# Optimization experiments

Measured on AMD Instinct MI355X. Metric: run time of the kernel, lower is better.

Reference implementation:

```python
import jax, jax.numpy as jnp
import numpy as np

B, S, D, H = 2, 2048, 1024, 16
HD = D // H  # 64


def setup_inputs() -> dict:
    key = jax.random.key(0)
    ks = jax.random.split(key, 10)
    inp = {
        "queries": jax.random.normal(ks[0], (B, S, D), dtype=jnp.float32),
        "keys": jax.random.normal(ks[1], (B, S, D), dtype=jnp.float32),
        "values": jax.random.normal(ks[2], (B, S, D), dtype=jnp.float32),
        "attention_mask": jax.random.randint(ks[3], (B, S), 0, 2, dtype=jnp.int32),
        # Linear params (torch nn.Linear: y = x @ W.T + b), scaled like default init
        "Wq": jax.random.normal(ks[4], (D, D), dtype=jnp.float32) / np.sqrt(D),
        "bq": jnp.zeros((D,), dtype=jnp.float32),
        "Wk": jax.random.normal(ks[5], (D, D), dtype=jnp.float32) / np.sqrt(D),
        "bk": jnp.zeros((D,), dtype=jnp.float32),
        "Wv": jax.random.normal(ks[6], (D, D), dtype=jnp.float32) / np.sqrt(D),
        "bv": jnp.zeros((D,), dtype=jnp.float32),
    }
    return inp


def _split_heads(x):
    # torch.chunk along last dim + stack(dim=1) == reshape + transpose
    b, s, d = x.shape
    return x.reshape(b, s, H, HD).transpose(0, 2, 1, 3)  # [B,H,S,hd]


def reference(queries, keys, values, attention_mask, Wq, bq, Wk, bk, Wv, bv):
    q = jax.nn.relu(queries @ Wq.T + bq)
    k = jax.nn.relu(keys @ Wk.T + bk)
    v = jax.nn.relu(values @ Wv.T + bv)
    qh, kh, vh = _split_heads(q), _split_heads(k), _split_heads(v)
    score = jnp.einsum("bhqd,bhkd->bhqk", qh, kh) / jnp.sqrt(jnp.float32(HD))
    # enc mask: [B,1,S,1] broadcast over key dim — masks whole query rows where mask==0
    row_mask = (attention_mask == 0)[:, None, :, None]
    score = jnp.where(row_mask, jnp.float32(-1e9), score)
    attn = jax.nn.softmax(score, axis=-1)
    a = jnp.einsum("bhqk,bhkd->bhqd", attn, vh)  # [B,H,S,hd]
    # faithful to original: permute(0,1,3,2) then reshape to (B,S,D)
    a = a.transpose(0, 1, 3, 2).reshape(q.shape[0], q.shape[1], q.shape[2])
    return a + queries
```

## Files before the change

### kernel.cpp

```cpp
#include <hip/hip_runtime.h>
#include <hip/hip_bf16.h>

#define DEV __device__ __forceinline__

typedef __attribute__((ext_vector_type(8))) short short8;
typedef __attribute__((ext_vector_type(4))) float f32x4;

#define MFMA16(a, b, c) __builtin_amdgcn_mfma_f32_16x16x32_bf16((a), (b), (c), 0, 0, 0)

static constexpr int B_ = 2, S_ = 2048, D_ = 1024, H_ = 16, HD_ = 64;
static constexpr long NX = (long)B_ * S_ * D_;
static constexpr long NW = (long)D_ * D_;

DEV short f2bf(float f) {
    __hip_bfloat16 h = __float2bfloat16(f);
    union { __hip_bfloat16 hh; short s; } u;
    u.hh = h;
    return u.s;
}

DEV float bf2f(short s) {
    union { float f; unsigned u; } x;
    x.u = ((unsigned)(unsigned short)s) << 16;
    return x.f;
}

DEV unsigned pk2(float a, float b) {
    union { float f; unsigned u; } ua, ub;
    ua.f = a; ub.f = b;
    return ((ua.u + 0x8000u) >> 16) | ((ub.u + 0x8000u) & 0xffff0000u);
}

DEV short8 ld8(const short* p) { return *(const short8*)p; }

DEV void gld16(const short* g, short* l) {
    __builtin_amdgcn_global_load_lds(
        (const __attribute__((address_space(1))) unsigned int*)g,
        (__attribute__((address_space(3))) unsigned int*)l, 16, 0, 0);
}

__global__ __launch_bounds__(256) void convert_all(
    const float* __restrict__ q, const float* __restrict__ k, const float* __restrict__ v,
    const float* __restrict__ wq, const float* __restrict__ wk, const float* __restrict__ wv,
    short* __restrict__ qb, short* __restrict__ kb, short* __restrict__ vb,
    short* __restrict__ wqb, short* __restrict__ wkb, short* __restrict__ wvb) {
    long tid = (long)blockIdx.x * 256 + threadIdx.x;
    long e = tid * 4;
    const float* src; short* dst; long off;
    if      (e < NX)            { src = q;  dst = qb;  off = e; }
    else if (e < 2*NX)          { src = k;  dst = kb;  off = e - NX; }
    else if (e < 3*NX)          { src = v;  dst = vb;  off = e - 2*NX; }
    else if (e < 3*NX + NW)     { src = wq; dst = wqb; off = e - 3*NX; }
    else if (e < 3*NX + 2*NW)   { src = wk; dst = wkb; off = e - 3*NX - NW; }
    else                        { src = wv; dst = wvb; off = e - 3*NX - 2*NW; }
    float4 f = *(const float4*)(src + off);
    short4 o;
    o.x = f2bf(f.x); o.y = f2bf(f.y); o.z = f2bf(f.z); o.w = f2bf(f.w);
    *(short4*)(dst + off) = o;
}

__global__ __launch_bounds__(256) void gemm_bias_relu(
    const short* __restrict__ X0, const short* __restrict__ X1, const short* __restrict__ X2,
    const short* __restrict__ W0, const short* __restrict__ W1, const short* __restrict__ W2,
    const float* __restrict__ b0, const float* __restrict__ b1, const float* __restrict__ b2,
    short* __restrict__ O0, short* __restrict__ O1, short* __restrict__ O2) {
    __shared__ short As[2][128 * 32];
    __shared__ short Bs[2][128 * 32];

    const int z = blockIdx.z;
    const short* X   = (z == 0) ? X0 : (z == 1) ? X1 : X2;
    const short* W   = (z == 0) ? W0 : (z == 1) ? W1 : W2;
    const float* bia = (z == 0) ? b0 : (z == 1) ? b1 : b2;
    short*       Out = (z == 0) ? O0 : (z == 1) ? O1 : O2;

    const int tid  = threadIdx.x;
    const int wid  = tid >> 6;
    const int lane = tid & 63;
    const int id   = lane & 15;
    const int quad = lane >> 4;
    const int m0 = blockIdx.y * 128;
    const int n0 = blockIdx.x * 128;
    const int wm = (wid >> 1) * 64;
    const int wn = (wid & 1) * 64;

    const short* Ag0 = X + (long)(m0 + wid * 32 + (lane >> 2)) * D_ + (lane & 3) * 8;
    const short* Bg0 = W + (long)(n0 + wid * 32 + (lane >> 2)) * D_ + (lane & 3) * 8;
    const int offW = wid * 1024;

    f32x4 acc[4][4] = {};

    gld16(Ag0,            &As[0][offW]);
    gld16(Ag0 + 16 * D_,  &As[0][offW + 512]);
    gld16(Bg0,            &Bs[0][offW]);
    gld16(Bg0 + 16 * D_,  &Bs[0][offW + 512]);

    for (int kk = 0; kk < D_; kk += 32) {
        const int cur = (kk >> 5) & 1;
        __syncthreads();
        if (kk + 32 < D_) {
            const int nxt = cur ^ 1;
            gld16(Ag0 + kk + 32,            &As[nxt][offW]);
            gld16(Ag0 + 16 * D_ + kk + 32,  &As[nxt][offW + 512]);
            gld16(Bg0 + kk + 32,            &Bs[nxt][offW]);
            gld16(Bg0 + 16 * D_ + kk + 32,  &Bs[nxt][offW + 512]);
        }

        short8 af[4], bf[4];
#pragma unroll
        for (int i = 0; i < 4; i++) af[i] = ld8(&As[cur][(wm + 16*i + id) * 32 + quad * 8]);
#pragma unroll
        for (int j = 0; j < 4; j++) bf[j] = ld8(&Bs[cur][(wn + 16*j + id) * 32 + quad * 8]);
#pragma unroll
        for (int i = 0; i < 4; i++)
#pragma unroll
            for (int j = 0; j < 4; j++)
                acc[i][j] = MFMA16(af[i], bf[j], acc[i][j]);
    }

#pragma unroll
    for (int j = 0; j < 4; j++) {
        int col = n0 + wn + 16*j + id;
        float bj = bia[col];
#pragma unroll
        for (int i = 0; i < 4; i++) {
#pragma unroll
            for (int r = 0; r < 4; r++) {
                int row = m0 + wm + 16*i + quad*4 + r;
                float val = fmaxf(acc[i][j][r] + bj, 0.f);
                Out[(long)row * D_ + col] = f2bf(val);
            }
        }
    }
}

__global__ __launch_bounds__(256) void transpose_v(const short* __restrict__ Vp,
                                                   short* __restrict__ VT) {
    __shared__ short tile[64 * 64];
    const int bh = blockIdx.y;
    const int b = bh >> 4, h = bh & 15;
    const int s0 = blockIdx.x * 64;
    const int t = threadIdx.x;
#pragma unroll
    for (int it = 0; it < 2; it++) {
        int row = (t >> 3) + 32 * it;
        int u   = t & 7;
        short8 d = ld8(Vp + (long)(b * S_ + s0 + row) * D_ + h * HD_ + u * 8);
        *(short8*)(&tile[row * 64 + (u ^ ((row >> 3) & 7)) * 8]) = d;
    }
    __syncthreads();
#pragma unroll
    for (int it = 0; it < 2; it++) {
        int e  = (t >> 3) + 32 * it;
        int sb = (t & 7) * 8;
        short8 o;
#pragma unroll
        for (int u = 0; u < 8; u++) {
            int row = sb + u;
            o[u] = tile[row * 64 + (((e >> 3) ^ ((row >> 3) & 7)) * 8) + (e & 7)];
        }
        *(short8*)(VT + ((long)bh * HD_ + e) * S_ + s0 + sb) = o;
    }
}

__global__ __launch_bounds__(256, 2) void attention(
    const short* __restrict__ Qb, const short* __restrict__ Kb,
    const short* __restrict__ VT, const int* __restrict__ mask,
    const float* __restrict__ queries, float* __restrict__ out) {
    __shared__ short Ks[2][64 * 64];
    __shared__ short Vs[2][64 * 64];
    __shared__ short pl[4][2 * 16 * 72];

    const int tid  = threadIdx.x;
    const int wid  = tid >> 6;
    const int lane = tid & 63;
    const int id   = lane & 15;
    const int quad = lane >> 4;

    const int bid = blockIdx.x;
    const int w   = bid >> 3;
    const int bh  = (bid & 7) + 8 * (w & 3);
    const int qt  = w >> 2;
    const int b   = bh >> 4;
    const int h   = bh & 15;
    const int q0  = qt * 128 + wid * 32;

    short8 qf[2][2];
#pragma unroll
    for (int g = 0; g < 2; g++) {
        const short* qbase = Qb + (long)(b * S_ + q0 + g * 16 + id) * D_ + h * HD_ + quad * 8;
        short8 f0 = ld8(qbase);
        short8 f1 = ld8(qbase + 32);
        const float qsc = mask[b * S_ + q0 + g * 16 + id] ? 0.125f : 0.f;
#pragma unroll
        for (int i = 0; i < 8; i++) {
            f0[i] = f2bf(bf2f(f0[i]) * qsc);
            f1[i] = f2bf(bf2f(f1[i]) * qsc);
        }
        qf[g][0] = f0; qf[g][1] = f1;
    }

    const int srow = wid * 16 + (lane >> 3);
    const int su   = (lane & 7) ^ (srow & 7);
    const short* kg0 = Kb + ((long)b * S_ + srow) * D_ + h * HD_ + su * 8;
    const short* vg0 = VT + (((long)(b * H_ + h) * HD_) + srow) * S_ + su * 8;
    short* plw = pl[wid];

    const int swz = id & 7;

    float l4[2][4] = {};
    f32x4 o[2][4] = {};

    gld16(kg0,            &Ks[0][wid * 1024]);
    gld16(kg0 + 8 * D_,   &Ks[0][wid * 1024 + 512]);
    gld16(vg0,            &Vs[0][wid * 1024]);
    gld16(vg0 + 8 * S_,   &Vs[0][wid * 1024 + 512]);

    for (int c0 = 0; c0 < S_; c0 += 64) {
        const int cur = (c0 >> 6) & 1;
        __syncthreads();
        if (c0 + 64 < S_) {
            const int nxt = cur ^ 1;
            const long cg = (long)(c0 + 64);
            gld16(kg0 + cg * D_,           &Ks[nxt][wid * 1024]);
            gld16(kg0 + cg * D_ + 8 * D_,  &Ks[nxt][wid * 1024 + 512]);
            gld16(vg0 + cg,                &Vs[nxt][wid * 1024]);
            gld16(vg0 + cg + 8 * S_,       &Vs[nxt][wid * 1024 + 512]);
        }

        f32x4 s[2][4];
#pragma unroll
        for (int g = 0; g < 2; g++)
#pragma unroll
            for (int t = 0; t < 4; t++) s[g][t] = (f32x4){0.f, 0.f, 0.f, 0.f};
#pragma unroll
        for (int t = 0; t < 4; t++) {
            short8 a0 = ld8(&Ks[cur][(16*t + id) * 64 + ((quad    ) ^ swz) * 8]);
            short8 a1 = ld8(&Ks[cur][(16*t + id) * 64 + ((quad ^ 4) ^ swz) * 8]);
            s[0][t] = MFMA16(a0, qf[0][0], s[0][t]);
            s[0][t] = MFMA16(a1, qf[0][1], s[0][t]);
            s[1][t] = MFMA16(a0, qf[1][0], s[1][t]);
            s[1][t] = MFMA16(a1, qf[1][1], s[1][t]);
        }

#pragma unroll
        for (int g = 0; g < 2; g++) {
            short* plg = plw + g * (16 * 72);
#pragma unroll
            for (int t = 0; t < 4; t++) {
                float p0 = __expf(s[g][t][0]);
                float p1 = __expf(s[g][t][1]);
                float p2 = __expf(s[g][t][2]);
                float p3 = __expf(s[g][t][3]);
                l4[g][0] += p0; l4[g][1] += p1; l4[g][2] += p2; l4[g][3] += p3;
                uint2 w2;
                w2.x = pk2(p0, p1);
                w2.y = pk2(p2, p3);
                *(uint2*)(&plg[id * 72 + 16 * t + quad * 4]) = w2;
            }
        }
        short8 pf[2][2];
#pragma unroll
        for (int g = 0; g < 2; g++) {
            short* plg = plw + g * (16 * 72);
            pf[g][0] = ld8(&plg[id * 72 + quad * 8]);
            pf[g][1] = ld8(&plg[id * 72 + 32 + quad * 8]);
        }

#pragma unroll
        for (int j2 = 0; j2 < 4; j2++) {
#pragma unroll
            for (int kh = 0; kh < 2; kh++) {
                short8 va = ld8(&Vs[cur][(16*j2 + id) * 64 + (((kh << 2) + quad) ^ swz) * 8]);
                o[0][j2] = MFMA16(va, pf[0][kh], o[0][j2]);
                o[1][j2] = MFMA16(va, pf[1][kh], o[1][j2]);
            }
        }
    }

    const long obase = (long)b * (S_ * D_) + (long)h * (HD_ * S_);
#pragma unroll
    for (int g = 0; g < 2; g++) {
        float l = l4[g][0] + l4[g][1] + l4[g][2] + l4[g][3];
        l += __shfl_xor(l, 16);
        l += __shfl_xor(l, 32);
        const float linv = 1.f / l;
#pragma unroll
        for (int j2 = 0; j2 < 4; j2++) {
#pragma unroll
            for (int r = 0; r < 4; r++) {
                int dim = 16 * j2 + quad * 4 + r;
                long idx = obase + (long)dim * S_ + q0 + g * 16 + id;
                out[idx] = o[g][j2][r] * linv + queries[idx];
            }
        }
    }
}

extern "C" void kernel_launch(void* const* d_in, const int* in_sizes, int n_in,
                              void* d_out, int out_size, void* d_ws, size_t ws_size,
                              hipStream_t stream) {
    const float* queries = (const float*)d_in[0];
    const float* keys    = (const float*)d_in[1];
    const float* values  = (const float*)d_in[2];
    const int*   mask    = (const int*)d_in[3];
    const float* Wq = (const float*)d_in[4];
    const float* bq = (const float*)d_in[5];
    const float* Wk = (const float*)d_in[6];
    const float* bk = (const float*)d_in[7];
    const float* Wv = (const float*)d_in[8];
    const float* bv = (const float*)d_in[9];
    float* out = (float*)d_out;

    short* ws  = (short*)d_ws;
    short* qb  = ws;
    short* kb  = qb  + NX;
    short* vb  = kb  + NX;
    short* wqb = vb  + NX;
    short* wkb = wqb + NW;
    short* wvb = wkb + NW;
    short* Q   = wvb + NW;
    short* K   = Q   + NX;
    short* Vp  = K   + NX;
    short* VT  = Vp  + NX;

    convert_all<<<15360, 256, 0, stream>>>(queries, keys, values, Wq, Wk, Wv,
                                           qb, kb, vb, wqb, wkb, wvb);
    gemm_bias_relu<<<dim3(8, 32, 3), 256, 0, stream>>>(qb, kb, vb, wqb, wkb, wvb,
                                                       bq, bk, bv, Q, K, Vp);
    transpose_v<<<dim3(32, 32), 256, 0, stream>>>(Vp, VT);
    attention<<<512, 256, 0, stream>>>(Q, K, VT, mask, queries, out);
}
```

Measured before the change: 203.3 us.

## Fuse V transpose into projection GEMM epilogue and vectorize output stores

The V projection GEMM now writes its output directly in the transposed per-head VT layout, which removes the separate transpose_v kernel and its extra global round trip. For Q and K, the MFMA operands are swapped so each lane holds four consecutive output columns and can issue 8-byte vectorized stores with float4 bias loads. The VT-path stores are short4 writes along the sequence dimension, strided across rows, and a per-z branch inside the K loop adds some divergence-free control overhead.

```diff
diff --git a/kernel.cpp b/kernel.cpp
--- a/kernel.cpp
+++ b/kernel.cpp
@@ -63,7 +63,7 @@
     const short* __restrict__ X0, const short* __restrict__ X1, const short* __restrict__ X2,
     const short* __restrict__ W0, const short* __restrict__ W1, const short* __restrict__ W2,
     const float* __restrict__ b0, const float* __restrict__ b1, const float* __restrict__ b2,
-    short* __restrict__ O0, short* __restrict__ O1, short* __restrict__ O2) {
+    short* __restrict__ O0, short* __restrict__ O1, short* __restrict__ VT) {
     __shared__ short As[2][128 * 32];
     __shared__ short Bs[2][128 * 32];
 
@@ -71,7 +71,6 @@
     const short* X   = (z == 0) ? X0 : (z == 1) ? X1 : X2;
     const short* W   = (z == 0) ? W0 : (z == 1) ? W1 : W2;
     const float* bia = (z == 0) ? b0 : (z == 1) ? b1 : b2;
-    short*       Out = (z == 0) ? O0 : (z == 1) ? O1 : O2;
 
     const int tid  = threadIdx.x;
     const int wid  = tid >> 6;
@@ -94,6 +93,8 @@
     gld16(Bg0,            &Bs[0][offW]);
     gld16(Bg0 + 16 * D_,  &Bs[0][offW + 512]);
 
+    const bool swap = (z != 2);
+
     for (int kk = 0; kk < D_; kk += 32) {
         const int cur = (kk >> 5) & 1;
         __syncthreads();
@@ -110,55 +111,56 @@
         for (int i = 0; i < 4; i++) af[i] = ld8(&As[cur][(wm + 16*i + id) * 32 + quad * 8]);
 #pragma unroll
         for (int j = 0; j < 4; j++) bf[j] = ld8(&Bs[cur][(wn + 16*j + id) * 32 + quad * 8]);
-#pragma unroll
-        for (int i = 0; i < 4; i++)
-#pragma unroll
-            for (int j = 0; j < 4; j++)
-                acc[i][j] = MFMA16(af[i], bf[j], acc[i][j]);
-    }
-
-#pragma unroll
-    for (int j = 0; j < 4; j++) {
-        int col = n0 + wn + 16*j + id;
-        float bj = bia[col];
+        if (swap) {
+#pragma unroll
+            for (int i = 0; i < 4; i++)
+#pragma unroll
+                for (int j = 0; j < 4; j++)
+                    acc[i][j] = MFMA16(bf[j], af[i], acc[i][j]);
+        } else {
+#pragma unroll
+            for (int i = 0; i < 4; i++)
+#pragma unroll
+                for (int j = 0; j < 4; j++)
+                    acc[i][j] = MFMA16(af[i], bf[j], acc[i][j]);
+        }
+    }
+
+    if (swap) {
+        short* Out = (z == 0) ? O0 : O1;
 #pragma unroll
         for (int i = 0; i < 4; i++) {
-#pragma unroll
-            for (int r = 0; r < 4; r++) {
-                int row = m0 + wm + 16*i + quad*4 + r;
-                float val = fmaxf(acc[i][j][r] + bj, 0.f);
-                Out[(long)row * D_ + col] = f2bf(val);
-            }
-        }
-    }
-}
-
-__global__ __launch_bounds__(256) void transpose_v(const short* __restrict__ Vp,
-                                                   short* __restrict__ VT) {
-    __shared__ short tile[64 * 64];
-    const int bh = blockIdx.y;
-    const int b = bh >> 4, h = bh & 15;
-    const int s0 = blockIdx.x * 64;
-    const int t = threadIdx.x;
-#pragma unroll
-    for (int it = 0; it < 2; it++) {
-        int row = (t >> 3) + 32 * it;
-        int u   = t & 7;
-        short8 d = ld8(Vp + (long)(b * S_ + s0 + row) * D_ + h * HD_ + u * 8);
-        *(short8*)(&tile[row * 64 + (u ^ ((row >> 3) & 7)) * 8]) = d;
-    }
-    __syncthreads();
-#pragma unroll
-    for (int it = 0; it < 2; it++) {
-        int e  = (t >> 3) + 32 * it;
-        int sb = (t & 7) * 8;
-        short8 o;
-#pragma unroll
-        for (int u = 0; u < 8; u++) {
-            int row = sb + u;
-            o[u] = tile[row * 64 + (((e >> 3) ^ ((row >> 3) & 7)) * 8) + (e & 7)];
-        }
-        *(short8*)(VT + ((long)bh * HD_ + e) * S_ + s0 + sb) = o;
+            const int m = m0 + wm + 16*i + id;
+#pragma unroll
+            for (int j = 0; j < 4; j++) {
+                const int nb = n0 + wn + 16*j + quad*4;
+                float4 bj = *(const float4*)(bia + nb);
+                short4 o4;
+                o4.x = f2bf(fmaxf(acc[i][j][0] + bj.x, 0.f));
+                o4.y = f2bf(fmaxf(acc[i][j][1] + bj.y, 0.f));
+                o4.z = f2bf(fmaxf(acc[i][j][2] + bj.z, 0.f));
+                o4.w = f2bf(fmaxf(acc[i][j][3] + bj.w, 0.f));
+                *(short4*)(Out + (long)m * D_ + nb) = o4;
+            }
+        }
+    } else {
+        const int b = m0 >> 11;
+#pragma unroll
+        for (int j = 0; j < 4; j++) {
+            const int n = n0 + wn + 16*j + id;
+            const float bj = bia[n];
+            const long vtb = ((long)(b * H_ + (n >> 6)) * HD_ + (n & 63)) * S_;
+#pragma unroll
+            for (int i = 0; i < 4; i++) {
+                const int s = ((m0 + wm + 16*i + quad*4) & (S_ - 1));
+                short4 o4;
+                o4.x = f2bf(fmaxf(acc[i][j][0] + bj, 0.f));
+                o4.y = f2bf(fmaxf(acc[i][j][1] + bj, 0.f));
+                o4.z = f2bf(fmaxf(acc[i][j][2] + bj, 0.f));
+                o4.w = f2bf(fmaxf(acc[i][j][3] + bj, 0.f));
+                *(short4*)(VT + vtb + s) = o4;
+            }
+        }
     }
 }
 
@@ -320,13 +322,11 @@
     short* wvb = wkb + NW;
     short* Q   = wvb + NW;
     short* K   = Q   + NX;
-    short* Vp  = K   + NX;
-    short* VT  = Vp  + NX;
+    short* VT  = K   + NX;
 
     convert_all<<<15360, 256, 0, stream>>>(queries, keys, values, Wq, Wk, Wv,
                                            qb, kb, vb, wqb, wkb, wvb);
     gemm_bias_relu<<<dim3(8, 32, 3), 256, 0, stream>>>(qb, kb, vb, wqb, wkb, wvb,
-                                                       bq, bk, bv, Q, K, Vp);
-    transpose_v<<<dim3(32, 32), 256, 0, stream>>>(Vp, VT);
+                                                       bq, bk, bv, Q, K, VT);
     attention<<<512, 256, 0, stream>>>(Q, K, VT, mask, queries, out);
 }
```

After: 241.1 us. +18.6%, slower.
